# Kernel optimization log

Measured on AMD Instinct MI355X. Metric: run time of the kernel, lower is better.

The kernel has to match this reference:

```python
import jax, jax.numpy as jnp
import numpy as np

B, T, C = 4, 4096, 1024
H = 16
D = C // H
EPS = 1e-06


def setup_inputs() -> dict:
    key = jax.random.key(0)
    k1, k2, k3 = jax.random.split(key, 3)
    x = jax.random.normal(k1, (B, T, C), dtype=jnp.float32)
    Wqkv = jax.random.normal(k2, (3 * C, C), dtype=jnp.float32) * (1.0 / np.sqrt(C))
    Wproj = jax.random.normal(k3, (C, C), dtype=jnp.float32) * (1.0 / np.sqrt(C))
    bproj = jnp.zeros((C,), dtype=jnp.float32)
    return {"x": x, "Wqkv": Wqkv, "Wproj": Wproj, "bproj": bproj}


def _phi(x):
    # elu(x) + 1 kernel feature map (non-negative)
    return jax.nn.elu(x) + 1.0


def reference(x, Wqkv, Wproj, bproj):
    b, t, c = x.shape
    qkv = jnp.einsum('btc,ec->bte', x, Wqkv)              # (B,T,3C)
    qkv = qkv.reshape(b, t, 3, H, D)
    q, k, v = qkv[:, :, 0], qkv[:, :, 1], qkv[:, :, 2]     # (B,T,H,D)
    q = _phi(q)
    k = _phi(k)
    # kv state: sum over sequence of outer products k_d v_m -> (B,H,D,D)
    kv = jnp.einsum('bnhd,bnhm->bhdm', k, v)
    k_sum = k.sum(axis=1)                                  # (B,H,D)
    out = jnp.einsum('bnhd,bhdm->bnhm', q, kv)             # (B,T,H,D)
    normalizer = jnp.einsum('bnhd,bhd->bnh', q, k_sum) + EPS
    out = out / normalizer[..., None]
    out = out.reshape(b, t, c)
    out = jnp.einsum('btc,oc->bto', out, Wproj) + bproj
    return out
```

## Files before the change

kernel.cpp:

```cpp
#include <hip/hip_runtime.h>

typedef __bf16 bf16;
typedef bf16 bf16x8 __attribute__((ext_vector_type(8)));
typedef bf16 bf16x4 __attribute__((ext_vector_type(4)));
typedef float f32x4 __attribute__((ext_vector_type(4)));

#define B_ 4
#define T_ 4096
#define C_ 1024
#define EPS_ 1e-6f
#define KVTSTR 16448

typedef __attribute__((address_space(1))) const void* as1p;
typedef __attribute__((address_space(3))) void* as3p;

__global__ void cast_kernel(const float* __restrict__ in, bf16* __restrict__ out, int n8) {
  int i = blockIdx.x * blockDim.x + threadIdx.x;
  int stride = gridDim.x * blockDim.x;
  for (; i < n8; i += stride) {
    const float4* p = (const float4*)(in + (size_t)i * 8);
    float4 v0 = p[0];
    float4 v1 = p[1];
    bf16x8 o;
    o[0] = (bf16)v0.x; o[1] = (bf16)v0.y; o[2] = (bf16)v0.z; o[3] = (bf16)v0.w;
    o[4] = (bf16)v1.x; o[5] = (bf16)v1.y; o[6] = (bf16)v1.z; o[7] = (bf16)v1.w;
    *(bf16x8*)(out + (size_t)i * 8) = o;
  }
}

#define BM 256
#define BN 256
#define BK 64
#define KD 1024
#define NTI (KD / BK)
#define TILB 32768
#define BUFB (2 * TILB)
#define SMEMB (2 * BUFB)

#define STG(p, ko, dst) __builtin_amdgcn_global_load_lds((as1p)((p) + (ko)), (as3p)(dst), 16, 0, 0)

#define LDA(MI0)                                                                       \
  _Pragma("unroll") for (int a = 0; a < 2; a++)                                        \
    _Pragma("unroll") for (int kk = 0; kk < 2; kk++)                                   \
      af[a][kk] = *(const bf16x8*)(Ab + (wm * 128 + ((MI0) + a) * 16 + fr) * 64 + swz[kk]);

#define MM(MI0)                                                                        \
  __builtin_amdgcn_s_setprio(1);                                                       \
  _Pragma("unroll") for (int a = 0; a < 2; a++)                                        \
    _Pragma("unroll") for (int nj = 0; nj < 4; nj++)                                   \
      _Pragma("unroll") for (int kk = 0; kk < 2; kk++)                                 \
        acc[(MI0) + a][nj] = __builtin_amdgcn_mfma_f32_16x16x32_bf16(af[a][kk], bfr[nj][kk], acc[(MI0) + a][nj], 0, 0, 0); \
  __builtin_amdgcn_s_setprio(0);

#define BAR1 { __builtin_amdgcn_s_barrier(); asm volatile("s_waitcnt lgkmcnt(0)" ::: "memory"); __builtin_amdgcn_sched_barrier(0); }
#define BAR2 { __builtin_amdgcn_s_barrier(); __builtin_amdgcn_sched_barrier(0); }

template <int MODE>
__global__ __launch_bounds__(512, 1) void gemm9(
    const bf16* __restrict__ A, const bf16* __restrict__ Bm,
    void* __restrict__ Cout, const float* __restrict__ bias,
    bf16* __restrict__ kvt, int M, int N, int tiles_n) {
  extern __shared__ char smem[];
  const int tid = threadIdx.x;
  const int l = tid & 63;
  const int w = tid >> 6;
  const int wm = w >> 2;
  const int wn = w & 3;

  const int cpx = gridDim.x >> 3;
  const int bid = (blockIdx.x & 7) * cpx + (blockIdx.x >> 3);
  const int tm = (bid / tiles_n) * BM;
  const int tn = (bid % tiles_n) * BN;

  const int gsw = ((tid & 7) ^ ((tid >> 3) & 7)) * 8;
  const int tsr = tid >> 3;

  const bf16* pA0 = A + (size_t)(tm + tsr) * KD + gsw;
  const bf16* pA1 = A + (size_t)(tm + 64 + tsr) * KD + gsw;
  const bf16* pA2 = A + (size_t)(tm + 128 + tsr) * KD + gsw;
  const bf16* pA3 = A + (size_t)(tm + 192 + tsr) * KD + gsw;
  const bf16* pB0 = Bm + (size_t)(tn + tsr) * KD + gsw;
  const bf16* pB1 = Bm + (size_t)(tn + 64 + tsr) * KD + gsw;
  const bf16* pB2 = Bm + (size_t)(tn + 128 + tsr) * KD + gsw;
  const bf16* pB3 = Bm + (size_t)(tn + 192 + tsr) * KD + gsw;

  const int fr = l & 15;
  const int fc = l >> 4;
  int swz[2];
  swz[0] = ((0 * 4 + fc) ^ (fr & 7)) * 8;
  swz[1] = ((1 * 4 + fc) ^ (fr & 7)) * 8;

  f32x4 acc[8][4] = {};

  STG(pA0, 0, smem + tid * 16);
  STG(pA1, 0, smem + 8192 + tid * 16);
  STG(pA2, 0, smem + 16384 + tid * 16);
  STG(pA3, 0, smem + 24576 + tid * 16);
  STG(pB0, 0, smem + TILB + tid * 16);
  STG(pB1, 0, smem + TILB + 8192 + tid * 16);
  STG(pB2, 0, smem + TILB + 16384 + tid * 16);
  STG(pB3, 0, smem + TILB + 24576 + tid * 16);
  asm volatile("s_waitcnt vmcnt(0)" ::: "memory");
  __builtin_amdgcn_s_barrier();
  __builtin_amdgcn_sched_barrier(0);

  for (int t = 0; t < NTI; ++t) {
    const bf16* Ab = (const bf16*)(smem + (t & 1) * BUFB);
    const bf16* Bb = (const bf16*)(smem + (t & 1) * BUFB + TILB);
    char* sd = smem + ((t & 1) ^ 1) * BUFB;
    const bool st = (t + 1 < NTI);
    const int ko = (t + 1) * BK;
    bf16x8 bfr[4][2], af[2][2];

#pragma unroll
    for (int nj = 0; nj < 4; nj++)
#pragma unroll
      for (int kk = 0; kk < 2; kk++)
        bfr[nj][kk] = *(const bf16x8*)(Bb + (wn * 64 + nj * 16 + fr) * 64 + swz[kk]);
    LDA(0)
    if (st) {
      STG(pB0, ko, sd + TILB + tid * 16);
      STG(pB1, ko, sd + TILB + 8192 + tid * 16);
      STG(pB2, ko, sd + TILB + 16384 + tid * 16);
      STG(pB3, ko, sd + TILB + 24576 + tid * 16);
    }
    BAR1 MM(0) BAR2

    LDA(2)
    if (st) {
      STG(pA0, ko, sd + tid * 16);
      STG(pA1, ko, sd + 8192 + tid * 16);
      STG(pA2, ko, sd + 16384 + tid * 16);
      STG(pA3, ko, sd + 24576 + tid * 16);
    }
    BAR1 MM(2) BAR2

    LDA(4)
    BAR1 MM(4) BAR2

    LDA(6)
    BAR1 MM(6)
    asm volatile("s_waitcnt vmcnt(0)" ::: "memory");
    BAR2
  }

  const int crow0 = tm + wm * 128 + (l >> 4) * 4;
  const int ccol0 = tn + wn * 64 + (l & 15);
  if (MODE == 0) {
    if (tn < 1024) {
      bf16* qbuf = (bf16*)Cout;
#pragma unroll
      for (int mi = 0; mi < 8; mi++)
#pragma unroll
        for (int nj = 0; nj < 4; nj++) {
          const int col = ccol0 + nj * 16;
#pragma unroll
          for (int r = 0; r < 4; r++) {
            const int row = crow0 + mi * 16 + r;
            float v = acc[mi][nj][r];
            v = (v > 0.f) ? (v + 1.0f) : __expf(v);
            qbuf[(size_t)row * 1024 + col] = (bf16)v;
          }
        }
    } else {
#pragma unroll
      for (int mi = 0; mi < 8; mi++)
#pragma unroll
        for (int nj = 0; nj < 4; nj++) {
          const int colp = ccol0 + nj * 16 - 1024;
          const bool isk = (colp < 1024);
          bf16x4 pk;
#pragma unroll
          for (int r = 0; r < 4; r++) {
            float v = acc[mi][nj][r];
            if (isk) v = (v > 0.f) ? (v + 1.0f) : __expf(v);
            pk[r] = (bf16)v;
          }
          const int n0 = crow0 + mi * 16;
          *(bf16x4*)(kvt + (size_t)colp * KVTSTR + n0) = pk;
        }
    }
  } else {
    float* Cf = (float*)Cout;
#pragma unroll
    for (int mi = 0; mi < 8; mi++)
#pragma unroll
      for (int nj = 0; nj < 4; nj++) {
        const int col = ccol0 + nj * 16;
        const float bv = bias[col];
#pragma unroll
        for (int r = 0; r < 4; r++) {
          const int row = crow0 + mi * 16 + r;
          Cf[(size_t)row * N + col] = acc[mi][nj][r] + bv;
        }
      }
  }
}

__global__ __launch_bounds__(256) void kvgemm(const bf16* __restrict__ kvt,
                                              float* __restrict__ partial) {
  const int kc = blockIdx.x >> 6;
  const int bh = blockIdx.x & 63;
  const int b = bh >> 4, h = bh & 15;
  const int l = threadIdx.x & 63;
  const int w = threadIdx.x >> 6;

  const size_t nb = (size_t)b * 4096 + kc * 1024 + (l >> 4) * 8;
  const bf16* Ar = kvt + (size_t)(h * 64 + w * 16 + (l & 15)) * KVTSTR + nb;
  const bf16* Br = kvt + (size_t)(1024 + h * 64 + (l & 15)) * KVTSTR + nb;

  f32x4 acc[4] = {};
  float ks = 0.f;
  bf16x8 aC, bC[4], aN, bN[4];
  aC = *(const bf16x8*)Ar;
#pragma unroll
  for (int nj = 0; nj < 4; nj++) bC[nj] = *(const bf16x8*)(Br + (size_t)nj * 16 * KVTSTR);

  for (int it = 0; it < 32; ++it) {
    if (it + 1 < 32) {
      aN = *(const bf16x8*)(Ar + (it + 1) * 32);
#pragma unroll
      for (int nj = 0; nj < 4; nj++)
        bN[nj] = *(const bf16x8*)(Br + (size_t)nj * 16 * KVTSTR + (it + 1) * 32);
    }
#pragma unroll
    for (int i = 0; i < 8; i++) ks += (float)aC[i];
#pragma unroll
    for (int nj = 0; nj < 4; nj++)
      acc[nj] = __builtin_amdgcn_mfma_f32_16x16x32_bf16(aC, bC[nj], acc[nj], 0, 0, 0);
    aC = aN;
#pragma unroll
    for (int nj = 0; nj < 4; nj++) bC[nj] = bN[nj];
  }

  ks += __shfl_xor(ks, 16);
  ks += __shfl_xor(ks, 32);

  float* p = partial + (size_t)(kc * 64 + bh) * 4160;
#pragma unroll
  for (int nj = 0; nj < 4; nj++) {
    const int m = nj * 16 + (l & 15);
#pragma unroll
    for (int r = 0; r < 4; r++) {
      const int d = w * 16 + (l >> 4) * 4 + r;
      p[d * 64 + m] = acc[nj][r];
    }
  }
  if (l < 16) p[4096 + w * 16 + l] = ks;
}

__global__ void kv_finalize(const float* __restrict__ partial, bf16* __restrict__ kvb) {
  const int bh = blockIdx.x;
  for (int i = threadIdx.x; i < 80 * 64; i += 256) {
    const int row = i >> 6;
    const int dd = i & 63;
    float outv = 0.f;
    if (row < 64) {
      float s = 0.f;
#pragma unroll
      for (int kc = 0; kc < 4; kc++)
        s += partial[(size_t)(kc * 64 + bh) * 4160 + dd * 64 + row];
      outv = s;
    } else if (row < 66) {
      float s = 0.f;
#pragma unroll
      for (int kc = 0; kc < 4; kc++)
        s += partial[(size_t)(kc * 64 + bh) * 4160 + 4096 + dd];
      bf16 hi = (bf16)s;
      outv = (row == 64) ? (float)hi : (s - (float)hi);
    }
    kvb[(size_t)bh * 5120 + row * 64 + dd] = (bf16)outv;
  }
}

__global__ __launch_bounds__(256) void attn_mfma(const bf16* __restrict__ qbuf,
                                                 const bf16* __restrict__ kvb,
                                                 bf16* __restrict__ attn) {
  const int bh = blockIdx.x >> 4;
  const int tch = blockIdx.x & 15;
  const int b = bh >> 4;
  const int h = bh & 15;
  const int lane = threadIdx.x & 63;
  const int wave = threadIdx.x >> 6;
  const int t0 = tch * 256 + wave * 64;

  const bf16* kvp = kvb + (size_t)bh * 5120;
  bf16x8 bfrag[5][2];
#pragma unroll
  for (int j = 0; j < 5; j++)
#pragma unroll
    for (int kk = 0; kk < 2; kk++)
      bfrag[j][kk] = *(const bf16x8*)(kvp + (j * 16 + (lane & 15)) * 64 + kk * 32 + (lane >> 4) * 8);

  f32x4 acc[4][5] = {};
#pragma unroll
  for (int i = 0; i < 4; i++) {
    const int t = t0 + i * 16 + (lane & 15);
    const bf16* qp = qbuf + (size_t)(b * T_ + t) * 1024 + h * 64 + (lane >> 4) * 8;
    bf16x8 a0 = *(const bf16x8*)qp;
    bf16x8 a1 = *(const bf16x8*)(qp + 32);
#pragma unroll
    for (int j = 0; j < 5; j++) {
      acc[i][j] = __builtin_amdgcn_mfma_f32_16x16x32_bf16(a0, bfrag[j][0], acc[i][j], 0, 0, 0);
      acc[i][j] = __builtin_amdgcn_mfma_f32_16x16x32_bf16(a1, bfrag[j][1], acc[i][j], 0, 0, 0);
    }
  }

#pragma unroll
  for (int i = 0; i < 4; i++) {
#pragma unroll
    for (int r = 0; r < 4; r++) {
      float hi = __shfl(acc[i][4][r], (lane & 48));
      float lo = __shfl(acc[i][4][r], (lane & 48) + 1);
      float inv = 1.0f / (hi + lo + EPS_);
      const int t = t0 + i * 16 + (lane >> 4) * 4 + r;
      bf16* op = attn + (size_t)(b * T_ + t) * 1024 + h * 64 + (lane & 15);
#pragma unroll
      for (int j = 0; j < 4; j++)
        op[j * 16] = (bf16)(acc[i][j][r] * inv);
    }
  }
}

extern "C" void kernel_launch(void* const* d_in, const int* in_sizes, int n_in,
                              void* d_out, int out_size, void* d_ws, size_t ws_size,
                              hipStream_t stream) {
  const float* x = (const float*)d_in[0];
  const float* Wqkv = (const float*)d_in[1];
  const float* Wproj = (const float*)d_in[2];
  const float* bproj = (const float*)d_in[3];
  float* out = (float*)d_out;

  char* w = (char*)d_ws;
  bf16* xw = (bf16*)w;      w += (size_t)16777216 * 2;
  bf16* wqkv = (bf16*)w;    w += (size_t)3145728 * 2;
  bf16* wproj = (bf16*)w;   w += (size_t)1048576 * 2;
  bf16* qbuf = (bf16*)w;    w += (size_t)16384 * 1024 * 2;
  bf16* kvt = (bf16*)w;     w += (size_t)2048 * KVTSTR * 2;
  bf16* attnb = (bf16*)w;   w += (size_t)16384 * 1024 * 2;
  float* partial = (float*)w; w += (size_t)4 * 64 * 4160 * 4;
  bf16* kvb = (bf16*)w;

  (void)hipFuncSetAttribute((const void*)gemm9<0>,
      hipFuncAttributeMaxDynamicSharedMemorySize, SMEMB);
  (void)hipFuncSetAttribute((const void*)gemm9<1>,
      hipFuncAttributeMaxDynamicSharedMemorySize, SMEMB);

  cast_kernel<<<8192, 256, 0, stream>>>(x, xw, 16777216 / 8);
  cast_kernel<<<1536, 256, 0, stream>>>(Wqkv, wqkv, 3145728 / 8);
  cast_kernel<<<512, 256, 0, stream>>>(Wproj, wproj, 1048576 / 8);

  gemm9<0><<<768, 512, SMEMB, stream>>>(xw, wqkv, (void*)qbuf, nullptr, kvt, 16384, 3072, 12);

  kvgemm<<<256, 256, 0, stream>>>(kvt, partial);
  kv_finalize<<<64, 256, 0, stream>>>(partial, kvb);

  attn_mfma<<<64 * 16, 256, 0, stream>>>(qbuf, kvb, attnb);

  gemm9<1><<<256, 512, SMEMB, stream>>>(attnb, wproj, (void*)out, bproj, nullptr, 16384, 1024, 4);
}
```

Measured before the change: 228.3 us.

## Use partial vmcnt waits in GEMM pipeline and merge the three cast kernels

New measurement: 221.1 us. 3.2% less time.

```diff
diff --git a/kernel.cpp b/kernel.cpp
--- a/kernel.cpp
+++ b/kernel.cpp
@@ -14,17 +14,26 @@
 typedef __attribute__((address_space(1))) const void* as1p;
 typedef __attribute__((address_space(3))) void* as3p;
 
-__global__ void cast_kernel(const float* __restrict__ in, bf16* __restrict__ out, int n8) {
+__global__ void cast_all(const float* __restrict__ x, const float* __restrict__ wq,
+                         const float* __restrict__ wp, bf16* __restrict__ xw,
+                         bf16* __restrict__ wqw, bf16* __restrict__ wpw) {
+  const int N0 = 16777216 / 8, N1 = 3145728 / 8, N2 = 1048576 / 8;
   int i = blockIdx.x * blockDim.x + threadIdx.x;
-  int stride = gridDim.x * blockDim.x;
-  for (; i < n8; i += stride) {
-    const float4* p = (const float4*)(in + (size_t)i * 8);
+  const int stride = gridDim.x * blockDim.x;
+  for (; i < N0 + N1 + N2; i += stride) {
+    const float* src;
+    bf16* dst;
+    int j;
+    if (i < N0) { src = x; dst = xw; j = i; }
+    else if (i < N0 + N1) { src = wq; dst = wqw; j = i - N0; }
+    else { src = wp; dst = wpw; j = i - N0 - N1; }
+    const float4* p = (const float4*)(src + (size_t)j * 8);
     float4 v0 = p[0];
     float4 v1 = p[1];
     bf16x8 o;
     o[0] = (bf16)v0.x; o[1] = (bf16)v0.y; o[2] = (bf16)v0.z; o[3] = (bf16)v0.w;
     o[4] = (bf16)v1.x; o[5] = (bf16)v1.y; o[6] = (bf16)v1.z; o[7] = (bf16)v1.w;
-    *(bf16x8*)(out + (size_t)i * 8) = o;
+    *(bf16x8*)(dst + (size_t)j * 8) = o;
   }
 }
 
@@ -56,7 +65,7 @@
 #define BAR2 { __builtin_amdgcn_s_barrier(); __builtin_amdgcn_sched_barrier(0); }
 
 template <int MODE>
-__global__ __launch_bounds__(512, 1) void gemm9(
+__global__ __launch_bounds__(512, 1) void gemmX(
     const bf16* __restrict__ A, const bf16* __restrict__ Bm,
     void* __restrict__ Cout, const float* __restrict__ bias,
     bf16* __restrict__ kvt, int M, int N, int tiles_n) {
@@ -92,15 +101,15 @@
 
   f32x4 acc[8][4] = {};
 
-  STG(pA0, 0, smem + tid * 16);
-  STG(pA1, 0, smem + 8192 + tid * 16);
-  STG(pA2, 0, smem + 16384 + tid * 16);
-  STG(pA3, 0, smem + 24576 + tid * 16);
   STG(pB0, 0, smem + TILB + tid * 16);
   STG(pB1, 0, smem + TILB + 8192 + tid * 16);
   STG(pB2, 0, smem + TILB + 16384 + tid * 16);
   STG(pB3, 0, smem + TILB + 24576 + tid * 16);
-  asm volatile("s_waitcnt vmcnt(0)" ::: "memory");
+  STG(pA0, 0, smem + tid * 16);
+  STG(pA2, 0, smem + 16384 + tid * 16);
+  STG(pA1, 0, smem + 8192 + tid * 16);
+  STG(pA3, 0, smem + 24576 + tid * 16);
+  asm volatile("s_waitcnt vmcnt(2)" ::: "memory");
   __builtin_amdgcn_s_barrier();
   __builtin_amdgcn_sched_barrier(0);
 
@@ -129,18 +138,21 @@
     LDA(2)
     if (st) {
       STG(pA0, ko, sd + tid * 16);
+      STG(pA2, ko, sd + 16384 + tid * 16);
       STG(pA1, ko, sd + 8192 + tid * 16);
-      STG(pA2, ko, sd + 16384 + tid * 16);
       STG(pA3, ko, sd + 24576 + tid * 16);
     }
-    BAR1 MM(2) BAR2
+    BAR1 MM(2)
+    if (st) { asm volatile("s_waitcnt vmcnt(8)" ::: "memory"); }
+    else    { asm volatile("s_waitcnt vmcnt(0)" ::: "memory"); }
+    BAR2
 
     LDA(4)
     BAR1 MM(4) BAR2
 
     LDA(6)
     BAR1 MM(6)
-    asm volatile("s_waitcnt vmcnt(0)" ::: "memory");
+    if (st) { asm volatile("s_waitcnt vmcnt(2)" ::: "memory"); }
     BAR2
   }
 
@@ -341,21 +353,19 @@
   float* partial = (float*)w; w += (size_t)4 * 64 * 4160 * 4;
   bf16* kvb = (bf16*)w;
 
-  (void)hipFuncSetAttribute((const void*)gemm9<0>,
+  (void)hipFuncSetAttribute((const void*)gemmX<0>,
       hipFuncAttributeMaxDynamicSharedMemorySize, SMEMB);
-  (void)hipFuncSetAttribute((const void*)gemm9<1>,
+  (void)hipFuncSetAttribute((const void*)gemmX<1>,
       hipFuncAttributeMaxDynamicSharedMemorySize, SMEMB);
 
-  cast_kernel<<<8192, 256, 0, stream>>>(x, xw, 16777216 / 8);
-  cast_kernel<<<1536, 256, 0, stream>>>(Wqkv, wqkv, 3145728 / 8);
-  cast_kernel<<<512, 256, 0, stream>>>(Wproj, wproj, 1048576 / 8);
-
-  gemm9<0><<<768, 512, SMEMB, stream>>>(xw, wqkv, (void*)qbuf, nullptr, kvt, 16384, 3072, 12);
+  cast_all<<<2048, 256, 0, stream>>>(x, Wqkv, Wproj, xw, wqkv, wproj);
+
+  gemmX<0><<<768, 512, SMEMB, stream>>>(xw, wqkv, (void*)qbuf, nullptr, kvt, 16384, 3072, 12);
 
   kvgemm<<<256, 256, 0, stream>>>(kvt, partial);
   kv_finalize<<<64, 256, 0, stream>>>(partial, kvb);
 
   attn_mfma<<<64 * 16, 256, 0, stream>>>(qbuf, kvb, attnb);
 
-  gemm9<1><<<256, 512, SMEMB, stream>>>(attnb, wproj, (void*)out, bproj, nullptr, 16384, 1024, 4);
-}
+  gemmX<1><<<256, 512, SMEMB, stream>>>(attnb, wproj, (void*)out, bproj, nullptr, 16384, 1024, 4);
+}
```
